# Performance work log

Hardware: AMD Instinct MI355X
Metric: run time of the kernel (lower is better)

The kernel has to match this reference:

```python
import jax, jax.numpy as jnp
import numpy as np

NUM_AA, EMB_DIM = 20, 16
H1, H2 = 128, 128
K, EXCLUDE = 64, 3
R_ON, R_CUT = 10.0, 12.0
RBF_CENTERS = (5.0, 6.0, 7.0, 8.0, 9.0, 10.0, 11.0)
RBF_WIDTH = 0.5
M = len(RBF_CENTERS)


def setup_inputs() -> dict:
    key = jax.random.key(0)
    ks = jax.random.split(key, 10)
    B, L = 8, 2048
    R = jax.random.normal(ks[0], (B, L, 3), dtype=jnp.float32) * 10.0  # spread distances over RBF range
    seq = jax.random.randint(ks[1], (B, L), 0, NUM_AA)
    emb_table = jax.random.normal(ks[2], (NUM_AA, EMB_DIM), dtype=jnp.float32) * 0.1
    in_dim = 3 * EMB_DIM
    W1 = jax.random.normal(ks[3], (in_dim, H1), dtype=jnp.float32) / np.sqrt(in_dim)
    b1 = jnp.zeros((H1,), jnp.float32)
    W2 = jax.random.normal(ks[4], (H1, H2), dtype=jnp.float32) / np.sqrt(H1)
    b2 = jnp.zeros((H2,), jnp.float32)
    W3 = jax.random.normal(ks[5], (H2, M), dtype=jnp.float32) / np.sqrt(H2)
    b3 = jnp.zeros((M,), jnp.float32)
    centers = jnp.asarray(RBF_CENTERS, jnp.float32)
    widths = jnp.full((M,), RBF_WIDTH, jnp.float32)
    return {"R": R, "seq": seq, "emb_table": emb_table,
            "W1": W1, "b1": b1, "W2": W2, "b2": b2, "W3": W3, "b3": b3,
            "centers": centers, "widths": widths}


def topk_nonbonded_pairs(R, K, exclude):
    # R: (B, L, 3) -> r: (B, L, K) distances, j: (B, L, K) neighbor indices
    B, L, _ = R.shape
    diff = R[:, :, None, :] - R[:, None, :, :]            # (B, L, L, 3)
    D = jnp.sqrt(jnp.sum(diff * diff, axis=-1) + 1e-12)   # (B, L, L)
    idx = jnp.arange(L)
    bonded = jnp.abs(idx[:, None] - idx[None, :]) <= exclude  # excludes self too
    D = jnp.where(bonded[None], jnp.inf, D)
    neg, j = jax.lax.top_k(-D, K)                          # K smallest distances
    return -neg, j


def smooth_switch(r, r_on, r_cut):
    t = jnp.clip((r - r_on) / (r_cut - r_on), 0.0, 1.0)
    return 1.0 - t * t * (3.0 - 2.0 * t)  # smoothstep down: 1 below r_on, 0 above r_cut


def distance_features(r, centers, widths):
    d = r[..., None] - centers  # (B, L, K, M)
    return jnp.exp(-(d * d) / (2.0 * widths * widths))


def reference(R, seq, emb_table, W1, b1, W2, b2, W3, b3, centers, widths):
    e = emb_table[seq]                                     # (B, L, d)
    r, j = topk_nonbonded_pairs(R, K, EXCLUDE)             # (B, L, K)
    e_j = jnp.take_along_axis(e[:, :, None, :], j[..., None], axis=1)  # wrong axis semantics avoided below
    # gather neighbor embeddings: e_j[b, i, k] = e[b, j[b, i, k]]
    e_j = jnp.take_along_axis(e[:, None, :, :].repeat(1, axis=1), j[..., None], axis=2) if False else \
          jnp.take_along_axis(e[:, :, None, :].transpose(0, 2, 1, 3).repeat(1, axis=0), j[..., None], axis=2) if False else \
          jax.vmap(lambda eb, jb: eb[jb])(e, j)            # (B, L, K, d)
    e_i = jnp.broadcast_to(e[:, :, None, :], e_j.shape)
    pair_feat = jnp.concatenate([e_i, e_j, e_i * e_j], axis=-1)  # (B, L, K, 3d)
    h = jax.nn.relu(pair_feat @ W1 + b1)
    h = jax.nn.relu(h @ W2 + b2)
    w = jax.nn.softplus(h @ W3 + b3)                       # (B, L, K, M)
    phi = distance_features(r, centers, widths)            # (B, L, K, M)
    att = -jnp.sum(w * phi, axis=-1)                       # (B, L, K)
    sw = smooth_switch(r, R_ON, R_CUT)
    return jnp.sum(att * sw, axis=(1, 2))                  # (B,)
```

## Files before the change

kernel.cpp:

```cpp
#include <hip/hip_runtime.h>
#include <math.h>

#define LSEQ 2048
#define KNB 64
#define BATCH 8
#define MRBF 7
#define NTILES 8192
#define NBLOCKS 768
#define BSCALE (255.0f/144.0f)

typedef __attribute__((ext_vector_type(8))) short short8;
typedef __attribute__((ext_vector_type(4))) float floatx4;

__device__ __forceinline__ unsigned short f2bf(float f) {
    unsigned u = __float_as_uint(f);
    u += 0x7fffu + ((u >> 16) & 1u);
    return (unsigned short)(u >> 16);
}
__device__ __forceinline__ unsigned pkbf(float a, float b) {
    return __builtin_amdgcn_perm(__float_as_uint(b) + 0x8000u,
                                 __float_as_uint(a) + 0x8000u, 0x07060302u);
}

__global__ __launch_bounds__(256) void fused_kernel(
    const float* __restrict__ R, const int* __restrict__ seq,
    const float* __restrict__ emb,
    const float* __restrict__ W1, const float* __restrict__ b1,
    const float* __restrict__ W2, const float* __restrict__ b2,
    const float* __restrict__ W3, const float* __restrict__ b3,
    const float* __restrict__ centers, const float* __restrict__ widths,
    float* __restrict__ out)
{
    __shared__ __align__(16) unsigned short lds[24832];
    int* nbrL = (int*)lds;
    unsigned short* Xs = lds + 256;
    unsigned short* Hs = lds + 8448;
    unsigned* hist    = (unsigned*)((char*)lds + 16896);
    float*    cand_d2 = (float*)((char*)lds + 18944);
    int*      cand_j  = (int*)((char*)lds + 19968);
    int*      tctr    = (int*)((char*)lds + 20992);
    int* sB    = tctr + 0;
    int* sNeed = tctr + 2;
    int* oPos  = tctr + 4;
    int* cCnt  = tctr + 6;
    int* fCnt  = tctr + 8;
    __shared__ float bacc[BATCH];

    const int tid  = threadIdx.x;
    const int lane = tid & 63;
    const int wv   = tid >> 6;
    const int l15  = lane & 15;
    const int q    = lane >> 4;

    short8 w1f[2][2], w2f[2][4], w3f[4];
    float b1v[2][4], b2v[2][4];
    #pragma unroll
    for (int mtl = 0; mtl < 2; mtl++) {
        int m = (2*wv + mtl)*16 + l15;
        #pragma unroll
        for (int d = 0; d < 4; d++) {
            b1v[mtl][d] = b1[(2*wv + mtl)*16 + q*4 + d];
            b2v[mtl][d] = b2[(2*wv + mtl)*16 + q*4 + d];
        }
        #pragma unroll
        for (int kt = 0; kt < 2; kt++)
            #pragma unroll
            for (int jj = 0; jj < 8; jj++) {
                int k = kt*32 + q*8 + jj;
                w1f[mtl][kt][jj] = (short)((k < 48) ? f2bf(W1[k*128 + m]) : 0);
            }
        #pragma unroll
        for (int kt = 0; kt < 4; kt++)
            #pragma unroll
            for (int jj = 0; jj < 8; jj++) {
                int k = kt*32 + q*8 + jj;
                w2f[mtl][kt][jj] = (short)f2bf(W2[k*128 + m]);
            }
    }
    #pragma unroll
    for (int kt = 0; kt < 4; kt++)
        #pragma unroll
        for (int jj = 0; jj < 8; jj++) {
            int k = kt*32 + q*8 + jj;
            w3f[kt][jj] = (short)((l15 < MRBF) ? f2bf(W3[k*MRBF + l15]) : 0);
        }
    float b3C[4], cen[4], i2w[4];
    #pragma unroll
    for (int d = 0; d < 4; d++) {
        int rb = q*4 + d;
        bool ok = rb < MRBF;
        b3C[d] = ok ? b3[rb] : 0.f;
        cen[d] = ok ? centers[rb] : 0.f;
        float wd = ok ? widths[rb] : 1.f;
        i2w[d] = 0.5f / (wd*wd);
    }
    if (tid < BATCH) bacc[tid] = 0.f;

    const int pl = tid >> 1, half = tid & 1;
    const int s7p = pl & 7;
    float rloc = 0.f;

    for (int tile = blockIdx.x; tile < NTILES; tile += NBLOCKS) {
        const int b     = tile >> 10;
        const int ibase = (tile & 1023) << 1;
        const float* Rb = R + ((b << 11) * 3);

        __syncthreads();

        hist[tid] = 0u; hist[tid + 256] = 0u;
        if (tid < 2) { oPos[tid] = 0; cCnt[tid] = 0; fCnt[tid] = 0; }

        float px[8], py[8], pz[8];
        {
            const float4* rp = (const float4*)(Rb + tid*24);
            float4 f0=rp[0], f1=rp[1], f2=rp[2], f3=rp[3], f4=rp[4], f5=rp[5];
            px[0]=f0.x; py[0]=f0.y; pz[0]=f0.z;
            px[1]=f0.w; py[1]=f1.x; pz[1]=f1.y;
            px[2]=f1.z; py[2]=f1.w; pz[2]=f2.x;
            px[3]=f2.y; py[3]=f2.z; pz[3]=f2.w;
            px[4]=f3.x; py[4]=f3.y; pz[4]=f3.z;
            px[5]=f3.w; py[5]=f4.x; pz[5]=f4.y;
            px[6]=f4.z; py[6]=f4.w; pz[6]=f5.x;
            px[7]=f5.y; py[7]=f5.z; pz[7]=f5.w;
        }
        float cx0 = Rb[3*ibase+0], cy0 = Rb[3*ibase+1], cz0 = Rb[3*ibase+2];
        float cx1 = Rb[3*ibase+3], cy1 = Rb[3*ibase+4], cz1 = Rb[3*ibase+5];
        __syncthreads();

        float d2r[2][8];
        #pragma unroll
        for (int u = 0; u < 8; u++) {
            int j = tid*8 + u;
            #pragma unroll
            for (int c = 0; c < 2; c++) {
                float dx = (c ? cx1 : cx0) - px[u];
                float dy = (c ? cy1 : cy0) - py[u];
                float dz = (c ? cz1 : cz0) - pz[u];
                float d2 = dx*dx + dy*dy + dz*dz;
                int dd = j - (ibase + c); dd = dd < 0 ? -dd : dd;
                if (dd <= 3) d2 = 1e30f;
                d2r[c][u] = d2;
                if (d2 < 144.0f)
                    atomicAdd(&hist[(c<<8) + (int)(d2*BSCALE)], 1u);
            }
        }
        __syncthreads();

        if (wv < 2) {
            unsigned h4[4]; unsigned s = 0;
            #pragma unroll
            for (int v = 0; v < 4; v++) { h4[v] = hist[(wv<<8) + lane*4 + v]; s += h4[v]; }
            unsigned inc = s;
            #pragma unroll
            for (int off = 1; off < 64; off <<= 1) {
                unsigned n = __shfl_up(inc, off, 64);
                if (lane >= off) inc += n;
            }
            unsigned tot = __shfl(inc, 63, 64);
            unsigned excl = inc - s;
            if (tot < 64u) {
                if (lane == 0) { sB[wv] = 255; sNeed[wv] = 64 - (int)tot; }
            } else if (excl < 64u && 64u <= inc) {
                unsigned cc = excl;
                #pragma unroll
                for (int v = 0; v < 4; v++) {
                    if (cc < 64u && 64u <= cc + h4[v]) { sB[wv] = lane*4+v; sNeed[wv] = 64 - (int)cc; }
                    cc += h4[v];
                }
            }
        }
        __syncthreads();

        #pragma unroll
        for (int u = 0; u < 8; u++) {
            int j = tid*8 + u;
            #pragma unroll
            for (int c = 0; c < 2; c++) {
                float d2 = d2r[c][u];
                int B = sB[c];
                if (d2 < 144.0f) {
                    int key = (int)(d2*BSCALE);
                    if (key < B) {
                        int pos = atomicAdd(&oPos[c], 1);
                        nbrL[(c<<6) + pos] = j;
                    } else if (key == B) {
                        int cc = atomicAdd(&cCnt[c], 1);
                        if (cc < 128) { cand_d2[(c<<7)+cc] = d2; cand_j[(c<<7)+cc] = j; }
                    }
                } else if (B == 255 && d2 < 1e29f) {
                    int t = atomicAdd(&fCnt[c], 1);
                    if (t < sNeed[c]) {
                        int pos = atomicAdd(&oPos[c], 1);
                        nbrL[(c<<6) + pos] = j;
                    }
                }
            }
        }
        __syncthreads();

        if (wv < 2) {
            int B = sB[wv];
            if (B != 255) {
                int cn = cCnt[wv]; if (cn > 128) cn = 128;
                int need = sNeed[wv];
                for (int ci = lane; ci < cn; ci += 64) {
                    float dv = cand_d2[(wv<<7)+ci]; int jv = cand_j[(wv<<7)+ci];
                    int rank = 0;
                    for (int x = 0; x < cn; x++) {
                        float dx2 = cand_d2[(wv<<7)+x]; int jx2 = cand_j[(wv<<7)+x];
                        rank += (dx2 < dv) || (dx2 == dv && jx2 < jv);
                    }
                    if (rank < need) {
                        int pos = atomicAdd(&oPos[wv], 1);
                        nbrL[(wv<<6) + pos] = jv;
                    }
                }
            }
        }
        __syncthreads();

        {
            int c  = pl >> 6;
            int bi = (b << 11) + ibase + c;
            int j  = nbrL[pl];
            int rowj = (b << 11) + j;
            int si = seq[bi], sj = seq[rowj];
            const float4* ei = (const float4*)(emb + si*16 + half*8);
            const float4* ej = (const float4*)(emb + sj*16 + half*8);
            float4 eA0 = ei[0], eA1 = ei[1], eB0 = ej[0], eB1 = ej[1];
            int rb = pl*64;
            uint4 vA = make_uint4(pkbf(eA0.x,eA0.y), pkbf(eA0.z,eA0.w),
                                  pkbf(eA1.x,eA1.y), pkbf(eA1.z,eA1.w));
            uint4 vB = make_uint4(pkbf(eB0.x,eB0.y), pkbf(eB0.z,eB0.w),
                                  pkbf(eB1.x,eB1.y), pkbf(eB1.z,eB1.w));
            uint4 vP = make_uint4(pkbf(eA0.x*eB0.x, eA0.y*eB0.y),
                                  pkbf(eA0.z*eB0.z, eA0.w*eB0.w),
                                  pkbf(eA1.x*eB1.x, eA1.y*eB1.y),
                                  pkbf(eA1.z*eB1.z, eA1.w*eB1.w));
            *(uint4*)&Xs[rb + (((0|half)^s7p)<<3)] = vA;
            *(uint4*)&Xs[rb + (((2|half)^s7p)<<3)] = vB;
            *(uint4*)&Xs[rb + (((4|half)^s7p)<<3)] = vP;
            *(uint4*)&Xs[rb + (((6|half)^s7p)<<3)] = make_uint4(0u,0u,0u,0u);
            if (!half) {
                float dx = R[bi*3+0]-R[rowj*3+0];
                float dy = R[bi*3+1]-R[rowj*3+1];
                float dz = R[bi*3+2]-R[rowj*3+2];
                rloc = sqrtf(dx*dx + dy*dy + dz*dz + 1e-12f);
            }
        }
        __syncthreads();

        #pragma unroll
        for (int nt = 0; nt < 8; nt++) {
            int row = nt*16 + l15;
            int s7 = l15 & 7;
            const unsigned short* xr = Xs + row*64;
            short8 x0 = *(const short8*)&xr[(( q    ^ s7) << 3)];
            short8 x1 = *(const short8*)&xr[(((4|q) ^ s7) << 3)];
            #pragma unroll
            for (int mtl = 0; mtl < 2; mtl++) {
                floatx4 acc = {b1v[mtl][0], b1v[mtl][1], b1v[mtl][2], b1v[mtl][3]};
                acc = __builtin_amdgcn_mfma_f32_16x16x32_bf16(w1f[mtl][0], x0, acc, 0, 0, 0);
                acc = __builtin_amdgcn_mfma_f32_16x16x32_bf16(w1f[mtl][1], x1, acc, 0, 0, 0);
                int chnk = (((2*wv + mtl)*2 + (q>>1)) ^ s7);
                *(uint2*)&Hs[row*128 + (chnk<<3) + ((q&1)<<2)] =
                    make_uint2(pkbf(fmaxf(acc[0],0.f), fmaxf(acc[1],0.f)),
                               pkbf(fmaxf(acc[2],0.f), fmaxf(acc[3],0.f)));
            }
        }
        __syncthreads();

        uint2 h2p[8][2];
        #pragma unroll
        for (int nt = 0; nt < 8; nt++) {
            int row = nt*16 + l15;
            int s7 = l15 & 7;
            const unsigned short* hr = Hs + row*128;
            short8 hf0 = *(const short8*)&hr[(( q     ^ s7) << 3)];
            short8 hf1 = *(const short8*)&hr[((( 4|q) ^ s7) << 3)];
            short8 hf2 = *(const short8*)&hr[((( 8|q) ^ s7) << 3)];
            short8 hf3 = *(const short8*)&hr[(((12|q) ^ s7) << 3)];
            #pragma unroll
            for (int mtl = 0; mtl < 2; mtl++) {
                floatx4 acc = {b2v[mtl][0], b2v[mtl][1], b2v[mtl][2], b2v[mtl][3]};
                acc = __builtin_amdgcn_mfma_f32_16x16x32_bf16(w2f[mtl][0], hf0, acc, 0, 0, 0);
                acc = __builtin_amdgcn_mfma_f32_16x16x32_bf16(w2f[mtl][1], hf1, acc, 0, 0, 0);
                acc = __builtin_amdgcn_mfma_f32_16x16x32_bf16(w2f[mtl][2], hf2, acc, 0, 0, 0);
                acc = __builtin_amdgcn_mfma_f32_16x16x32_bf16(w2f[mtl][3], hf3, acc, 0, 0, 0);
                h2p[nt][mtl] = make_uint2(pkbf(fmaxf(acc[0],0.f), fmaxf(acc[1],0.f)),
                                          pkbf(fmaxf(acc[2],0.f), fmaxf(acc[3],0.f)));
            }
        }
        __syncthreads();
        #pragma unroll
        for (int nt = 0; nt < 8; nt++) {
            int row = nt*16 + l15;
            int s7 = l15 & 7;
            #pragma unroll
            for (int mtl = 0; mtl < 2; mtl++) {
                int chnk = (((2*wv + mtl)*2 + (q>>1)) ^ s7);
                *(uint2*)&Hs[row*128 + (chnk<<3) + ((q&1)<<2)] = h2p[nt][mtl];
            }
        }
        __syncthreads();

        float esum = 0.f;
        #pragma unroll
        for (int ntl = 0; ntl < 2; ntl++) {
            int nt = 2*wv + ntl;
            int row = nt*16 + l15;
            int s7 = l15 & 7;
            const unsigned short* hr = Hs + row*128;
            floatx4 a3 = {b3C[0], b3C[1], b3C[2], b3C[3]};
            #pragma unroll
            for (int kt = 0; kt < 4; kt++) {
                short8 hf = *(const short8*)&hr[((((kt<<2)|q) ^ s7) << 3)];
                a3 = __builtin_amdgcn_mfma_f32_16x16x32_bf16(w3f[kt], hf, a3, 0, 0, 0);
            }
            float rr = __shfl(rloc, (ntl<<5) + 2*l15, 64);
            if (rr < 12.0f) {
                float att = 0.f;
                #pragma unroll
                for (int d = 0; d < 4; d++) {
                    if (q*4 + d < MRBF) {
                        float x = a3[d];
                        float sp = fmaxf(x, 0.f) + __logf(1.f + __expf(-fabsf(x)));
                        float df = rr - cen[d];
                        att += sp * __expf(-df*df*i2w[d]);
                    }
                }
                att += __shfl_xor(att, 16, 64);
                att += __shfl_xor(att, 32, 64);
                float t = fminf(fmaxf((rr - 10.f)*0.5f, 0.f), 1.f);
                float sw = 1.f - t*t*(3.f - 2.f*t);
                esum -= att * sw;
            }
        }
        #pragma unroll
        for (int off = 1; off < 64; off <<= 1)
            esum += __shfl_xor(esum, off, 64);
        if (lane == 0) atomicAdd(&bacc[b], esum * 0.25f);
    }
    __syncthreads();
    if (tid < BATCH) atomicAdd(&out[tid], bacc[tid]);
}

extern "C" void kernel_launch(void* const* d_in, const int* in_sizes, int n_in,
                              void* d_out, int out_size, void* d_ws, size_t ws_size,
                              hipStream_t stream) {
    const float* R       = (const float*)d_in[0];
    const int*   seq     = (const int*)  d_in[1];
    const float* emb     = (const float*)d_in[2];
    const float* W1      = (const float*)d_in[3];
    const float* b1      = (const float*)d_in[4];
    const float* W2      = (const float*)d_in[5];
    const float* b2      = (const float*)d_in[6];
    const float* W3      = (const float*)d_in[7];
    const float* b3      = (const float*)d_in[8];
    const float* centers = (const float*)d_in[9];
    const float* widths  = (const float*)d_in[10];
    float* out = (float*)d_out;

    hipMemsetAsync(d_out, 0, out_size * sizeof(float), stream);

    fused_kernel<<<NBLOCKS, 256, 0, stream>>>(R, seq, emb, W1, b1, W2, b2, W3, b3,
                                              centers, widths, out);
}
```

Before: 295.8 us.

## Software-pipeline next tile's neighbor selection into current tile's MLP phases

Restructures the tile loop so that the distance computation, histogram, threshold scan, candidate compaction and rank selection for the next tile are interleaved with the MLP layers of the current tile. Neighbor lists are double-buffered in LDS, and the candidate arrays are aliased onto the Xs region. The grid shrinks from 768 to 512 blocks to fit the larger LDS footprint. The aim is to hide global loads and selection latency behind MFMA work and to remove a barrier. The cost is higher register pressure and fewer resident blocks. Aliasing cand_d2/cand_j onto Xs risks a race if Xs is still being read when candidates are written.

Result: slower. 392.4 us (+32.6%).

```diff
diff --git a/kernel.cpp b/kernel.cpp
--- a/kernel.cpp
+++ b/kernel.cpp
@@ -6,7 +6,7 @@
 #define BATCH 8
 #define MRBF 7
 #define NTILES 8192
-#define NBLOCKS 768
+#define NBLOCKS 512
 #define BSCALE (255.0f/144.0f)
 
 typedef __attribute__((ext_vector_type(8))) short short8;
@@ -31,19 +31,19 @@
     const float* __restrict__ centers, const float* __restrict__ widths,
     float* __restrict__ out)
 {
-    __shared__ __align__(16) unsigned short lds[24832];
-    int* nbrL = (int*)lds;
-    unsigned short* Xs = lds + 256;
-    unsigned short* Hs = lds + 8448;
-    unsigned* hist    = (unsigned*)((char*)lds + 16896);
-    float*    cand_d2 = (float*)((char*)lds + 18944);
-    int*      cand_j  = (int*)((char*)lds + 19968);
-    int*      tctr    = (int*)((char*)lds + 20992);
+    __shared__ __align__(16) unsigned short lds[26136];
+    unsigned short* Xs = lds;
+    unsigned short* Hs = lds + 8192;
+    int*      nbrL = (int*)(lds + 24576);
+    unsigned* hist = (unsigned*)(lds + 25088);
+    int*      tctr = (int*)(lds + 26112);
     int* sB    = tctr + 0;
     int* sNeed = tctr + 2;
     int* oPos  = tctr + 4;
     int* cCnt  = tctr + 6;
     int* fCnt  = tctr + 8;
+    float* cand_d2 = (float*)lds;
+    int*   cand_j  = (int*)(lds + 512);
     __shared__ float bacc[BATCH];
 
     const int tid  = threadIdx.x;
@@ -98,36 +98,25 @@
 
     const int pl = tid >> 1, half = tid & 1;
     const int s7p = pl & 7;
-    float rloc = 0.f;
-
-    for (int tile = blockIdx.x; tile < NTILES; tile += NBLOCKS) {
-        const int b     = tile >> 10;
-        const int ibase = (tile & 1023) << 1;
-        const float* Rb = R + ((b << 11) * 3);
-
-        __syncthreads();
-
+
+    float d2r[2][8];
+
+    {
+        const int t0 = blockIdx.x;
         hist[tid] = 0u; hist[tid + 256] = 0u;
         if (tid < 2) { oPos[tid] = 0; cCnt[tid] = 0; fCnt[tid] = 0; }
-
+        __syncthreads();
+        const int ibn = (t0 & 1023) << 1;
+        const float* Rbn = R + (((t0 >> 10) << 11) * 3);
+        const float4* rp = (const float4*)(Rbn + tid*24);
+        float4 f0=rp[0], f1=rp[1], f2=rp[2], f3=rp[3], f4=rp[4], f5=rp[5];
+        float cx0 = Rbn[3*ibn+0], cy0 = Rbn[3*ibn+1], cz0 = Rbn[3*ibn+2];
+        float cx1 = Rbn[3*ibn+3], cy1 = Rbn[3*ibn+4], cz1 = Rbn[3*ibn+5];
         float px[8], py[8], pz[8];
-        {
-            const float4* rp = (const float4*)(Rb + tid*24);
-            float4 f0=rp[0], f1=rp[1], f2=rp[2], f3=rp[3], f4=rp[4], f5=rp[5];
-            px[0]=f0.x; py[0]=f0.y; pz[0]=f0.z;
-            px[1]=f0.w; py[1]=f1.x; pz[1]=f1.y;
-            px[2]=f1.z; py[2]=f1.w; pz[2]=f2.x;
-            px[3]=f2.y; py[3]=f2.z; pz[3]=f2.w;
-            px[4]=f3.x; py[4]=f3.y; pz[4]=f3.z;
-            px[5]=f3.w; py[5]=f4.x; pz[5]=f4.y;
-            px[6]=f4.z; py[6]=f4.w; pz[6]=f5.x;
-            px[7]=f5.y; py[7]=f5.z; pz[7]=f5.w;
-        }
-        float cx0 = Rb[3*ibase+0], cy0 = Rb[3*ibase+1], cz0 = Rb[3*ibase+2];
-        float cx1 = Rb[3*ibase+3], cy1 = Rb[3*ibase+4], cz1 = Rb[3*ibase+5];
-        __syncthreads();
-
-        float d2r[2][8];
+        px[0]=f0.x; py[0]=f0.y; pz[0]=f0.z;  px[1]=f0.w; py[1]=f1.x; pz[1]=f1.y;
+        px[2]=f1.z; py[2]=f1.w; pz[2]=f2.x;  px[3]=f2.y; py[3]=f2.z; pz[3]=f2.w;
+        px[4]=f3.x; py[4]=f3.y; pz[4]=f3.z;  px[5]=f3.w; py[5]=f4.x; pz[5]=f4.y;
+        px[6]=f4.z; py[6]=f4.w; pz[6]=f5.x;  px[7]=f5.y; py[7]=f5.z; pz[7]=f5.w;
         #pragma unroll
         for (int u = 0; u < 8; u++) {
             int j = tid*8 + u;
@@ -137,7 +126,7 @@
                 float dy = (c ? cy1 : cy0) - py[u];
                 float dz = (c ? cz1 : cz0) - pz[u];
                 float d2 = dx*dx + dy*dy + dz*dz;
-                int dd = j - (ibase + c); dd = dd < 0 ? -dd : dd;
+                int dd = j - (ibn + c); dd = dd < 0 ? -dd : dd;
                 if (dd <= 3) d2 = 1e30f;
                 d2r[c][u] = d2;
                 if (d2 < 144.0f)
@@ -145,7 +134,6 @@
             }
         }
         __syncthreads();
-
         if (wv < 2) {
             unsigned h4[4]; unsigned s = 0;
             #pragma unroll
@@ -170,7 +158,6 @@
             }
         }
         __syncthreads();
-
         #pragma unroll
         for (int u = 0; u < 8; u++) {
             int j = tid*8 + u;
@@ -197,7 +184,6 @@
             }
         }
         __syncthreads();
-
         if (wv < 2) {
             int B = sB[wv];
             if (B != 255) {
@@ -218,11 +204,24 @@
             }
         }
         __syncthreads();
-
+    }
+
+    int cur = 0;
+    for (int tile = blockIdx.x; tile < NTILES; tile += NBLOCKS) {
+        const int b   = tile >> 10;
+        const int tn  = tile + NBLOCKS;
+        const bool hn = tn < NTILES;
+        const int nxt = cur ^ 1;
+        float rloc = 0.f;
+
+        if (hn) {
+            hist[tid] = 0u; hist[tid + 256] = 0u;
+            if (tid < 2) { oPos[tid] = 0; cCnt[tid] = 0; fCnt[tid] = 0; }
+        }
         {
             int c  = pl >> 6;
-            int bi = (b << 11) + ibase + c;
-            int j  = nbrL[pl];
+            int bi = (b << 11) + ((tile & 1023) << 1) + c;
+            int j  = nbrL[cur*128 + pl];
             int rowj = (b << 11) + j;
             int si = seq[bi], sj = seq[rowj];
             const float4* ei = (const float4*)(emb + si*16 + half*8);
@@ -250,6 +249,17 @@
         }
         __syncthreads();
 
+        float4 f0, f1, f2, f3, f4, f5;
+        float cx0=0, cy0=0, cz0=0, cx1=0, cy1=0, cz1=0;
+        int ibn = 0;
+        if (hn) {
+            const float* Rbn = R + (((tn >> 10) << 11) * 3);
+            ibn = (tn & 1023) << 1;
+            const float4* rp = (const float4*)(Rbn + tid*24);
+            f0=rp[0]; f1=rp[1]; f2=rp[2]; f3=rp[3]; f4=rp[4]; f5=rp[5];
+            cx0 = Rbn[3*ibn+0]; cy0 = Rbn[3*ibn+1]; cz0 = Rbn[3*ibn+2];
+            cx1 = Rbn[3*ibn+3]; cy1 = Rbn[3*ibn+4]; cz1 = Rbn[3*ibn+5];
+        }
         #pragma unroll
         for (int nt = 0; nt < 8; nt++) {
             int row = nt*16 + l15;
@@ -268,6 +278,29 @@
                                pkbf(fmaxf(acc[2],0.f), fmaxf(acc[3],0.f)));
             }
         }
+        if (hn) {
+            float px[8], py[8], pz[8];
+            px[0]=f0.x; py[0]=f0.y; pz[0]=f0.z;  px[1]=f0.w; py[1]=f1.x; pz[1]=f1.y;
+            px[2]=f1.z; py[2]=f1.w; pz[2]=f2.x;  px[3]=f2.y; py[3]=f2.z; pz[3]=f2.w;
+            px[4]=f3.x; py[4]=f3.y; pz[4]=f3.z;  px[5]=f3.w; py[5]=f4.x; pz[5]=f4.y;
+            px[6]=f4.z; py[6]=f4.w; pz[6]=f5.x;  px[7]=f5.y; py[7]=f5.z; pz[7]=f5.w;
+            #pragma unroll
+            for (int u = 0; u < 8; u++) {
+                int j = tid*8 + u;
+                #pragma unroll
+                for (int c = 0; c < 2; c++) {
+                    float dx = (c ? cx1 : cx0) - px[u];
+                    float dy = (c ? cy1 : cy0) - py[u];
+                    float dz = (c ? cz1 : cz0) - pz[u];
+                    float d2 = dx*dx + dy*dy + dz*dz;
+                    int dd = j - (ibn + c); dd = dd < 0 ? -dd : dd;
+                    if (dd <= 3) d2 = 1e30f;
+                    d2r[c][u] = d2;
+                    if (d2 < 144.0f)
+                        atomicAdd(&hist[(c<<8) + (int)(d2*BSCALE)], 1u);
+                }
+            }
+        }
         __syncthreads();
 
         uint2 h2p[8][2];
@@ -291,7 +324,31 @@
                                           pkbf(fmaxf(acc[2],0.f), fmaxf(acc[3],0.f)));
             }
         }
-        __syncthreads();
+        if (hn && wv < 2) {
+            unsigned h4[4]; unsigned s = 0;
+            #pragma unroll
+            for (int v = 0; v < 4; v++) { h4[v] = hist[(wv<<8) + lane*4 + v]; s += h4[v]; }
+            unsigned inc = s;
+            #pragma unroll
+            for (int off = 1; off < 64; off <<= 1) {
+                unsigned n = __shfl_up(inc, off, 64);
+                if (lane >= off) inc += n;
+            }
+            unsigned tot = __shfl(inc, 63, 64);
+            unsigned excl = inc - s;
+            if (tot < 64u) {
+                if (lane == 0) { sB[wv] = 255; sNeed[wv] = 64 - (int)tot; }
+            } else if (excl < 64u && 64u <= inc) {
+                unsigned cc = excl;
+                #pragma unroll
+                for (int v = 0; v < 4; v++) {
+                    if (cc < 64u && 64u <= cc + h4[v]) { sB[wv] = lane*4+v; sNeed[wv] = 64 - (int)cc; }
+                    cc += h4[v];
+                }
+            }
+        }
+        __syncthreads();
+
         #pragma unroll
         for (int nt = 0; nt < 8; nt++) {
             int row = nt*16 + l15;
@@ -300,6 +357,33 @@
             for (int mtl = 0; mtl < 2; mtl++) {
                 int chnk = (((2*wv + mtl)*2 + (q>>1)) ^ s7);
                 *(uint2*)&Hs[row*128 + (chnk<<3) + ((q&1)<<2)] = h2p[nt][mtl];
+            }
+        }
+        if (hn) {
+            #pragma unroll
+            for (int u = 0; u < 8; u++) {
+                int j = tid*8 + u;
+                #pragma unroll
+                for (int c = 0; c < 2; c++) {
+                    float d2 = d2r[c][u];
+                    int B = sB[c];
+                    if (d2 < 144.0f) {
+                        int key = (int)(d2*BSCALE);
+                        if (key < B) {
+                            int pos = atomicAdd(&oPos[c], 1);
+                            nbrL[nxt*128 + (c<<6) + pos] = j;
+                        } else if (key == B) {
+                            int cc = atomicAdd(&cCnt[c], 1);
+                            if (cc < 128) { cand_d2[(c<<7)+cc] = d2; cand_j[(c<<7)+cc] = j; }
+                        }
+                    } else if (B == 255 && d2 < 1e29f) {
+                        int t = atomicAdd(&fCnt[c], 1);
+                        if (t < sNeed[c]) {
+                            int pos = atomicAdd(&oPos[c], 1);
+                            nbrL[nxt*128 + (c<<6) + pos] = j;
+                        }
+                    }
+                }
             }
         }
         __syncthreads();
@@ -336,12 +420,33 @@
                 esum -= att * sw;
             }
         }
+        if (hn && wv < 2) {
+            int B = sB[wv];
+            if (B != 255) {
+                int cn = cCnt[wv]; if (cn > 128) cn = 128;
+                int need = sNeed[wv];
+                for (int ci = lane; ci < cn; ci += 64) {
+                    float dv = cand_d2[(wv<<7)+ci]; int jv = cand_j[(wv<<7)+ci];
+                    int rank = 0;
+                    for (int x = 0; x < cn; x++) {
+                        float dx2 = cand_d2[(wv<<7)+x]; int jx2 = cand_j[(wv<<7)+x];
+                        rank += (dx2 < dv) || (dx2 == dv && jx2 < jv);
+                    }
+                    if (rank < need) {
+                        int pos = atomicAdd(&oPos[wv], 1);
+                        nbrL[nxt*128 + (wv<<6) + pos] = jv;
+                    }
+                }
+            }
+        }
         #pragma unroll
         for (int off = 1; off < 64; off <<= 1)
             esum += __shfl_xor(esum, off, 64);
         if (lane == 0) atomicAdd(&bacc[b], esum * 0.25f);
+        __syncthreads();
+
+        cur = nxt;
     }
-    __syncthreads();
     if (tid < BATCH) atomicAdd(&out[tid], bacc[tid]);
 }
 
```
